# Kernel tuning notes

Hardware: AMD Instinct MI355X
Metric: run time of the kernel (lower is better)

## Reference

```python
import jax, jax.numpy as jnp
import numpy as np

ALPHA = 0.1
BETA = 0.25


def setup_inputs() -> dict:
    key = jax.random.key(0)
    k1, k2 = jax.random.split(key)
    B, C, D = 65536, 4096, 128
    x = jax.random.normal(k1, (B, D), dtype=jnp.float32)
    codes = jax.random.normal(k2, (1, C, D), dtype=jnp.float32)
    return {"x": x, "codes": codes}


def reference(x, codes):
    # x: [B, D], codes: [1, C, D]
    D = x.shape[1]
    c = codes[0]  # [C, D]
    d2 = (
        jnp.sum(x * x, axis=1, keepdims=True)
        + jnp.sum(c * c, axis=1)[None, :]
        - 2.0 * (x @ c.T)
    )  # [B, C]
    distances = jnp.sqrt(jnp.maximum(d2, 0.0)) / (D ** 0.5) / ALPHA
    indices = jnp.argmin(distances, axis=-1)  # [B]
    quantized = c[indices]  # [B, D] codebook gather
    loss_commit = jnp.mean(
        jnp.sum((x - jax.lax.stop_gradient(quantized)) ** 2, axis=-1)
    )
    loss_codebook = jnp.mean(
        jnp.sum((quantized - jax.lax.stop_gradient(x)) ** 2, axis=-1)
    )
    loss = loss_commit + BETA * loss_codebook
    return quantized, indices, loss
```

## Files before the change

### kernel.cpp

```cpp
#include <hip/hip_runtime.h>

constexpr int Bn = 65536;
constexpr int Cn = 4096;
constexpr int Dn = 128;
constexpr float TAU = 0.055f;

typedef _Float16 v8h __attribute__((ext_vector_type(8)));
typedef float v16f __attribute__((ext_vector_type(16)));

#define MFMA16(a, b, c) __builtin_amdgcn_mfma_f32_32x32x16_f16((a), (b), (c), 0, 0, 0)

__global__ void pack_codes_kernel(const float* __restrict__ codes,
                                  float* __restrict__ cnorm,
                                  _Float16* __restrict__ pack,
                                  float* __restrict__ codesT,
                                  int* __restrict__ flagcount) {
  int tid = blockIdx.x * 256 + threadIdx.x;
  if (tid == 0) *flagcount = 0;
  int f = tid >> 6;
  int l = tid & 63;
  int ct = f / 9, s = f % 9;
  int code = (ct << 5) + (l & 31);
  if (s < 8) {
    int kb = (s << 4) + ((l >> 5) << 3);
    const float* p = codes + (size_t)code * Dn + kb;
    float4 a = ((const float4*)p)[0];
    float4 b = ((const float4*)p)[1];
    float v[8] = {a.x, a.y, a.z, a.w, b.x, b.y, b.z, b.w};
#pragma unroll
    for (int j = 0; j < 8; ++j)
      codesT[(size_t)(kb + j) * Cn + code] = v[j];
    v8h hi;
#pragma unroll
    for (int j = 0; j < 8; ++j) {
      float sv = -2.f * v[j];
      hi[j] = (_Float16)sv;
    }
    *(v8h*)(pack + (size_t)ct * 4608 + s * 512 + l * 8) = hi;
  } else {
    v8h a = {0, 0, 0, 0, 0, 0, 0, 0};
    if (l < 32) {
      const float4* p = (const float4*)(codes + (size_t)code * Dn);
      double sd = 0.0;
#pragma unroll
      for (int i = 0; i < Dn / 4; ++i) {
        float4 v = p[i];
        sd += (double)v.x * v.x + (double)v.y * v.y + (double)v.z * v.z +
              (double)v.w * v.w;
      }
      float cn = (float)sd;
      cnorm[code] = cn;
      float c5 = cn + 512.f;
      _Float16 h1 = (_Float16)c5;
      float r1 = c5 - (float)h1;
      _Float16 h2 = (_Float16)r1;
      float r2 = r1 - (float)h2;
      _Float16 h3 = (_Float16)r2;
      a[0] = h1;
      a[1] = h2;
      a[2] = h3;
    }
    *(v8h*)(pack + (size_t)ct * 4608 + 8 * 512 + l * 8) = a;
  }
}

__launch_bounds__(64, 2)
__global__ void argmin_mfma_kernel(const float* __restrict__ x,
                                   const _Float16* __restrict__ pack,
                                   float* __restrict__ pm1,
                                   float* __restrict__ pm2,
                                   float* __restrict__ pidx) {
  __shared__ __align__(16) _Float16 packLDS[2][4608];

  const int l = threadIdx.x;
  const int h = blockIdx.x & 3;
  const int row0 = (blockIdx.x >> 2) * 64;

  v8h xh[2][8];
#pragma unroll
  for (int tt = 0; tt < 2; ++tt) {
#pragma unroll
    for (int ks = 0; ks < 8; ++ks) {
      int xrow = row0 + tt * 32 + (l & 31);
      int kb = ks * 16 + (l >> 5) * 8;
      const float* xp = x + (size_t)xrow * Dn + kb;
      float4 a = ((const float4*)xp)[0];
      float4 b = ((const float4*)xp)[1];
      float v[8] = {a.x, a.y, a.z, a.w, b.x, b.y, b.z, b.w};
      v8h hh;
#pragma unroll
      for (int j = 0; j < 8; ++j) hh[j] = (_Float16)v[j];
      xh[tt][ks] = hh;
    }
  }

  v8h bones;
#pragma unroll
  for (int j = 0; j < 8; ++j)
    bones[j] = (l < 32 && j < 3) ? (_Float16)1.0f : (_Float16)0.0f;

  v16f zacc;
#pragma unroll
  for (int i = 0; i < 16; ++i) zacc[i] = 0.f;

  const char* packbase = (const char*)pack + (size_t)(h * 32) * 9216;
  auto stage = [&](int ct, int bufi) {
    const char* src = packbase + (size_t)ct * 9216 + l * 16;
    char* dstb = (char*)&packLDS[bufi][0];
#pragma unroll
    for (int i = 0; i < 9; ++i) {
      __builtin_amdgcn_global_load_lds(
          (const __attribute__((address_space(1))) unsigned*)(src + i * 1024),
          (__attribute__((address_space(3))) unsigned*)(dstb + i * 1024), 16,
          0, 0);
    }
  };

  stage(0, 0);

  unsigned umin1[2] = {0xFFFFFFFFu, 0xFFFFFFFFu};
  unsigned umin2[2] = {0xFFFFFFFFu, 0xFFFFFFFFu};
  int idx[2] = {0, 0};

  auto update = [&](const v16f& a, int tt, int codebase) {
    unsigned b[16];
#pragma unroll
    for (int r = 0; r < 16; ++r)
      b[r] = (__float_as_uint(a[r]) & 0xFFFFFFF0u) | (unsigned)r;
    unsigned m1 = 0xFFFFFFFFu, m2 = 0xFFFFFFFFu;
#pragma unroll
    for (int i = 0; i < 8; ++i) {
      unsigned lo = min(b[2 * i], b[2 * i + 1]);
      unsigned hi = max(b[2 * i], b[2 * i + 1]);
      unsigned mx = max(m1, lo);
      m1 = min(m1, lo);
      m2 = min(min(m2, hi), mx);
    }
    unsigned r1 = m1 & 15u;
    int tidx = codebase + (int)(8 * (r1 >> 2) + (r1 & 3));
    bool lt = m1 < umin1[tt];
    umin2[tt] = lt ? min(umin1[tt], m2) : min(umin2[tt], m1);
    idx[tt] = lt ? tidx : idx[tt];
    umin1[tt] = lt ? m1 : umin1[tt];
  };

  for (int it = 0; it < 32; ++it) {
    const int buf = it & 1;
    asm volatile("s_waitcnt vmcnt(0)" ::: "memory");
    if (it + 1 < 32) stage(it + 1, buf ^ 1);

    const _Float16* base = &packLDS[buf][l * 8];
    v8h a_cn = *(const v8h*)(base + 8 * 512);
    v16f ini = MFMA16(a_cn, bones, zacc);
    v8h a_h0 = *(const v8h*)(base + 0 * 512);
    v16f acc0 = MFMA16(a_h0, xh[0][0], ini);
    v16f acc1 = MFMA16(a_h0, xh[1][0], ini);
#pragma unroll
    for (int s = 1; s < 8; ++s) {
      v8h a_h = *(const v8h*)(base + s * 512);
      acc0 = MFMA16(a_h, xh[0][s], acc0);
      acc1 = MFMA16(a_h, xh[1][s], acc1);
    }
    const int codebase = h * 1024 + it * 32 + 4 * (l >> 5);
    update(acc0, 0, codebase);
    update(acc1, 1, codebase);
  }

#pragma unroll
  for (int tt = 0; tt < 2; ++tt) {
    unsigned o1 = (unsigned)__shfl_xor((int)umin1[tt], 32);
    unsigned o2 = (unsigned)__shfl_xor((int)umin2[tt], 32);
    int oi = __shfl_xor(idx[tt], 32);
    bool sw = (o1 < umin1[tt]) || (o1 == umin1[tt] && oi < idx[tt]);
    unsigned n1 = sw ? o1 : umin1[tt];
    int ni = sw ? oi : idx[tt];
    unsigned big = sw ? umin1[tt] : o1;
    unsigned n2 = min(min(umin2[tt], o2), big);
    if (l < 32) {
      int row = row0 + tt * 32 + l;
      pm1[h * Bn + row] = __uint_as_float(n1 & 0xFFFFFFF0u);
      pm2[h * Bn + row] = __uint_as_float(n2 & 0xFFFFFFF0u);
      pidx[h * Bn + row] = (float)ni;
    }
  }
}

__global__ void merge_kernel(const float* __restrict__ pm1,
                             const float* __restrict__ pm2,
                             const float* __restrict__ pidx,
                             float* __restrict__ idxf,
                             int* __restrict__ flaglist,
                             int* __restrict__ flagcount) {
  int r = blockIdx.x * 256 + threadIdx.x;
  float m1 = pm1[r];
  float mw2 = pm2[r];
  float mi = pidx[r];
  float m2 = 3.4e38f;
#pragma unroll
  for (int h = 1; h < 4; ++h) {
    float v1 = pm1[h * Bn + r];
    float v2 = pm2[h * Bn + r];
    float vi = pidx[h * Bn + r];
    bool win = v1 < m1;
    m2 = fminf(m2, win ? m1 : v1);
    mw2 = win ? v2 : mw2;
    mi = win ? vi : mi;
    m1 = win ? v1 : m1;
  }
  m2 = fminf(m2, mw2);
  idxf[r] = mi;
  if (m2 - m1 < TAU) {
    int p = atomicAdd(flagcount, 1);
    flaglist[p] = r;
  }
}

__launch_bounds__(256, 4)
__global__ void rescore_part_kernel(const float* __restrict__ x,
                                    const float* __restrict__ codesT,
                                    const float* __restrict__ cnorm,
                                    const int* __restrict__ flaglist,
                                    const int* __restrict__ flagcount,
                                    float* __restrict__ prv,
                                    int* __restrict__ pri) {
  __shared__ __align__(16) float xs[8][Dn];
  __shared__ float wv[4][8];
  __shared__ int wis[4][8];
  const int t = threadIdx.x;
  const int cnt = *flagcount;
  const int nb = (cnt + 7) >> 3;
  const int total = nb * 4;

  for (int wi = blockIdx.x; wi < total; wi += gridDim.x) {
    const int b = wi >> 2;
    const int q = wi & 3;
    __syncthreads();
    {
      int rr = t >> 5;
      int cc = t & 31;
      int j = min(b * 8 + rr, cnt - 1);
      int r = flaglist[j];
      ((float4*)&xs[rr][0])[cc] = ((const float4*)(x + (size_t)r * Dn))[cc];
    }
    __syncthreads();

    const int c0 = q * 1024 + 4 * t;
    const float* cp = codesT + c0;
    float4 s[8];
#pragma unroll
    for (int r = 0; r < 8; ++r) s[r] = (float4){0.f, 0.f, 0.f, 0.f};
    for (int d = 0; d < Dn; ++d) {
      float4 cv = *(const float4*)(cp + (size_t)d * Cn);
#pragma unroll
      for (int r = 0; r < 8; ++r) {
        float xv = xs[r][d];
        s[r].x = fmaf(cv.x, xv, s[r].x);
        s[r].y = fmaf(cv.y, xv, s[r].y);
        s[r].z = fmaf(cv.z, xv, s[r].z);
        s[r].w = fmaf(cv.w, xv, s[r].w);
      }
    }
    const float cn0 = cnorm[c0], cn1 = cnorm[c0 + 1], cn2 = cnorm[c0 + 2],
                cn3 = cnorm[c0 + 3];
    float bv[8];
    int bi[8];
#pragma unroll
    for (int r = 0; r < 8; ++r) {
      float k0 = fmaf(-2.f, s[r].x, cn0);
      float k1 = fmaf(-2.f, s[r].y, cn1);
      float k2 = fmaf(-2.f, s[r].z, cn2);
      float k3 = fmaf(-2.f, s[r].w, cn3);
      float v = k0;
      int i = c0;
      if (k1 < v) { v = k1; i = c0 + 1; }
      if (k2 < v) { v = k2; i = c0 + 2; }
      if (k3 < v) { v = k3; i = c0 + 3; }
      bv[r] = v;
      bi[r] = i;
    }
#pragma unroll
    for (int r = 0; r < 8; ++r) {
#pragma unroll
      for (int off = 32; off > 0; off >>= 1) {
        float ov = __shfl_down(bv[r], off);
        int oi = __shfl_down(bi[r], off);
        if (ov < bv[r] || (ov == bv[r] && oi < bi[r])) {
          bv[r] = ov;
          bi[r] = oi;
        }
      }
    }
    if ((t & 63) == 0) {
#pragma unroll
      for (int r = 0; r < 8; ++r) {
        wv[t >> 6][r] = bv[r];
        wis[t >> 6][r] = bi[r];
      }
    }
    __syncthreads();
    if (t < 8) {
      float v = wv[0][t];
      int i = wis[0][t];
#pragma unroll
      for (int k = 1; k < 4; ++k) {
        float ov = wv[k][t];
        int oi = wis[k][t];
        if (ov < v || (ov == v && oi < i)) { v = ov; i = oi; }
      }
      prv[wi * 8 + t] = v;
      pri[wi * 8 + t] = i;
    }
  }
}

__global__ void rescore_final_kernel(const int* __restrict__ flaglist,
                                     const int* __restrict__ flagcount,
                                     const float* __restrict__ prv,
                                     const int* __restrict__ pri,
                                     float* __restrict__ idxf) {
  const int cnt = *flagcount;
  for (int j = blockIdx.x * blockDim.x + threadIdx.x; j < cnt;
       j += gridDim.x * blockDim.x) {
    const int b = j >> 3;
    const int rr = j & 7;
    float bv = prv[(b * 4 + 0) * 8 + rr];
    int bi = pri[(b * 4 + 0) * 8 + rr];
#pragma unroll
    for (int k = 1; k < 4; ++k) {
      float ov = prv[(b * 4 + k) * 8 + rr];
      int oi = pri[(b * 4 + k) * 8 + rr];
      if (ov < bv || (ov == bv && oi < bi)) { bv = ov; bi = oi; }
    }
    idxf[flaglist[j]] = (float)bi;
  }
}

__global__ void gather_loss_kernel(const float* __restrict__ x,
                                   const float* __restrict__ codes,
                                   const float* __restrict__ idxf,
                                   float* __restrict__ quant,
                                   float* __restrict__ partial) {
  __shared__ float part[8];
  const int t = threadIdx.x;
  const int wave = t >> 6;
  const int lane = t & 63;
  const int half = lane >> 5;
  const int l = lane & 31;
  const int base = blockIdx.x * 32;

  float s = 0.f;
#pragma unroll
  for (int pass = 0; pass < 4; ++pass) {
    int row = base + pass * 8 + (wave << 1) + half;
    int idx = (int)idxf[row];
    float4 cv = ((const float4*)(codes + (size_t)idx * Dn))[l];
    float4 xv = ((const float4*)(x + (size_t)row * Dn))[l];
    ((float4*)(quant + (size_t)row * Dn))[l] = cv;
    float d0 = xv.x - cv.x, d1 = xv.y - cv.y, d2 = xv.z - cv.z,
          d3 = xv.w - cv.w;
    s += d0 * d0 + d1 * d1 + d2 * d2 + d3 * d3;
  }
#pragma unroll
  for (int off = 16; off > 0; off >>= 1) s += __shfl_down(s, off, 32);
  if (l == 0) part[(wave << 1) + half] = s;
  __syncthreads();
  if (t == 0) {
    float tot = 0.f;
#pragma unroll
    for (int i = 0; i < 8; ++i) tot += part[i];
    partial[blockIdx.x] = tot;
  }
}

__global__ void loss_sum_kernel(const float* __restrict__ partial,
                                float* __restrict__ loss) {
  __shared__ float red[4];
  const int t = threadIdx.x;
  float s = 0.f;
  for (int i = t; i < 2048; i += 256) s += partial[i];
#pragma unroll
  for (int off = 32; off > 0; off >>= 1) s += __shfl_down(s, off, 64);
  if ((t & 63) == 0) red[t >> 6] = s;
  __syncthreads();
  if (t == 0)
    *loss = (red[0] + red[1] + red[2] + red[3]) * (1.25f / 65536.f);
}

extern "C" void kernel_launch(void* const* d_in, const int* in_sizes, int n_in,
                              void* d_out, int out_size, void* d_ws,
                              size_t ws_size, hipStream_t stream) {
  const float* x = (const float*)d_in[0];
  const float* codes = (const float*)d_in[1];

  float* quant = (float*)d_out;
  float* idxf = quant + (size_t)Bn * Dn;
  float* loss = idxf + Bn;
  float* cnorm = (float*)d_ws;
  float* partial = cnorm + Cn;

  _Float16* pack = (_Float16*)quant;
  int* flagcount = (int*)(quant + (1 << 20));
  int* flaglist = flagcount + 1;
  float* pm1 = quant + (2 << 20);
  float* pm2 = pm1 + 4 * Bn;
  float* pidx = pm2 + 4 * Bn;
  float* codesT = quant + (3 << 20);
  float* prv = quant + (4 << 20);
  int* pri = (int*)(quant + (4 << 20) + (1 << 18));

  pack_codes_kernel<<<288, 256, 0, stream>>>(codes, cnorm, pack, codesT,
                                             flagcount);
  argmin_mfma_kernel<<<4096, 64, 0, stream>>>(x, pack, pm1, pm2, pidx);
  merge_kernel<<<Bn / 256, 256, 0, stream>>>(pm1, pm2, pidx, idxf, flaglist,
                                             flagcount);
  rescore_part_kernel<<<1024, 256, 0, stream>>>(x, codesT, cnorm, flaglist,
                                                flagcount, prv, pri);
  rescore_final_kernel<<<64, 256, 0, stream>>>(flaglist, flagcount, prv, pri,
                                               idxf);
  gather_loss_kernel<<<Bn / 32, 256, 0, stream>>>(x, codes, idxf, quant,
                                                  partial);
  loss_sum_kernel<<<1, 256, 0, stream>>>(partial, loss);
}
```

Baseline: 215.2 us.

## Load codebook fragments directly to registers with software-pipelined MFMA and argmin update

Drops the LDS double buffer fed by global_load_lds and instead loads each lane's packed fp16 codebook fragments straight from global memory into registers. Two register fragment sets alternate, so the next tile's loads and the previous tile's argmin update overlap with the current tile's MFMAs. This removes LDS traffic and the per-iteration vmcnt(0) wait, but raises VGPR pressure (two 9-fragment buffers plus four accumulators) and depends on L2 to serve the codebook reuse.

```diff
diff --git a/kernel.cpp b/kernel.cpp
--- a/kernel.cpp
+++ b/kernel.cpp
@@ -70,8 +70,6 @@
                                    float* __restrict__ pm1,
                                    float* __restrict__ pm2,
                                    float* __restrict__ pidx) {
-  __shared__ __align__(16) _Float16 packLDS[2][4608];
-
   const int l = threadIdx.x;
   const int h = blockIdx.x & 3;
   const int row0 = (blockIdx.x >> 2) * 64;
@@ -103,21 +101,6 @@
 #pragma unroll
   for (int i = 0; i < 16; ++i) zacc[i] = 0.f;
 
-  const char* packbase = (const char*)pack + (size_t)(h * 32) * 9216;
-  auto stage = [&](int ct, int bufi) {
-    const char* src = packbase + (size_t)ct * 9216 + l * 16;
-    char* dstb = (char*)&packLDS[bufi][0];
-#pragma unroll
-    for (int i = 0; i < 9; ++i) {
-      __builtin_amdgcn_global_load_lds(
-          (const __attribute__((address_space(1))) unsigned*)(src + i * 1024),
-          (__attribute__((address_space(3))) unsigned*)(dstb + i * 1024), 16,
-          0, 0);
-    }
-  };
-
-  stage(0, 0);
-
   unsigned umin1[2] = {0xFFFFFFFFu, 0xFFFFFFFFu};
   unsigned umin2[2] = {0xFFFFFFFFu, 0xFFFFFFFFu};
   int idx[2] = {0, 0};
@@ -144,27 +127,49 @@
     umin1[tt] = lt ? m1 : umin1[tt];
   };
 
-  for (int it = 0; it < 32; ++it) {
-    const int buf = it & 1;
-    asm volatile("s_waitcnt vmcnt(0)" ::: "memory");
-    if (it + 1 < 32) stage(it + 1, buf ^ 1);
-
-    const _Float16* base = &packLDS[buf][l * 8];
-    v8h a_cn = *(const v8h*)(base + 8 * 512);
-    v16f ini = MFMA16(a_cn, bones, zacc);
-    v8h a_h0 = *(const v8h*)(base + 0 * 512);
-    v16f acc0 = MFMA16(a_h0, xh[0][0], ini);
-    v16f acc1 = MFMA16(a_h0, xh[1][0], ini);
+  const _Float16* pb = pack + (size_t)(h * 32) * 4608 + l * 8;
+
+  auto loadf = [&](v8h* f, int it) {
+    const _Float16* tp = pb + (size_t)it * 4608;
+#pragma unroll
+    for (int s = 0; s < 8; ++s) f[s] = *(const v8h*)(tp + s * 512);
+    f[8] = *(const v8h*)(tp + 8 * 512);
+  };
+
+  auto mfma_tile = [&](const v8h* f, v16f& a0, v16f& a1) {
+    v16f ini = MFMA16(f[8], bones, zacc);
+    a0 = MFMA16(f[0], xh[0][0], ini);
+    a1 = MFMA16(f[0], xh[1][0], ini);
 #pragma unroll
     for (int s = 1; s < 8; ++s) {
-      v8h a_h = *(const v8h*)(base + s * 512);
-      acc0 = MFMA16(a_h, xh[0][s], acc0);
-      acc1 = MFMA16(a_h, xh[1][s], acc1);
-    }
-    const int codebase = h * 1024 + it * 32 + 4 * (l >> 5);
-    update(acc0, 0, codebase);
-    update(acc1, 1, codebase);
-  }
+      a0 = MFMA16(f[s], xh[0][s], a0);
+      a1 = MFMA16(f[s], xh[1][s], a1);
+    }
+  };
+
+  auto cb = [&](int t) { return h * 1024 + t * 32 + 4 * (l >> 5); };
+
+  v8h fA[9], fB[9];
+  v16f accA0, accA1, accB0, accB1;
+
+  loadf(fA, 0);
+  loadf(fB, 1);
+  mfma_tile(fA, accA0, accA1);
+  for (int it = 1; it < 31; it += 2) {
+    loadf(fA, it + 1);
+    mfma_tile(fB, accB0, accB1);
+    update(accA0, 0, cb(it - 1));
+    update(accA1, 1, cb(it - 1));
+    loadf(fB, it + 2);
+    mfma_tile(fA, accA0, accA1);
+    update(accB0, 0, cb(it));
+    update(accB1, 1, cb(it));
+  }
+  mfma_tile(fB, accB0, accB1);
+  update(accA0, 0, cb(30));
+  update(accA1, 1, cb(30));
+  update(accB0, 0, cb(31));
+  update(accB1, 1, cb(31));
 
 #pragma unroll
   for (int tt = 0; tt < 2; ++tt) {
```

Result: faster. 207.4 us (-3.6%).
